# Performance work log

Measured on AMD Instinct MI355X. Metric: run time of the kernel, lower is better.

The kernel has to match this reference:

```python
import jax, jax.numpy as jnp
import numpy as np

B, S, IN, OUT = 4, 2048, 4096, 11008


def setup_inputs() -> dict:
    key = jax.random.key(0)
    k1, k2, k3, k4, k5 = jax.random.split(key, 5)
    x = jax.random.normal(k1, (B, S, IN), dtype=jnp.float32)
    # int8 quantized weights, stored as int32 per harness spec but values in int8 range
    W_int8 = jax.random.randint(k2, (OUT, IN), -128, 128, dtype=jnp.int32)
    # per-output-channel scales (small positive) and zero-points
    scale = jax.random.uniform(k3, (OUT,), dtype=jnp.float32, minval=1e-3, maxval=2e-2)
    zero = jax.random.uniform(k4, (OUT,), dtype=jnp.float32, minval=-8.0, maxval=8.0)
    bias = jax.random.normal(k5, (OUT,), dtype=jnp.float32) * 0.01
    return {"x": x, "W_int8": W_int8, "scale": scale, "zero": zero, "bias": bias}


def reference(x, W_int8, scale, zero, bias):
    # Original torch forward raises on NaN/Inf in x; for valid inputs the math is
    # quant_matmul: dequantize W = (W_int8 - zero) * scale (per output channel),
    # then y = x @ W.T + bias.
    W = (W_int8.astype(jnp.float32) - zero[:, None]) * scale[:, None]  # [OUT, IN]
    y = jnp.einsum('bsi,oi->bso', x, W) + bias  # [B, S, OUT]
    return y
```

## Files before the change

### kernel.cpp

```cpp
#include <hip/hip_runtime.h>
#include <stdint.h>


#define M_DIM 8192
#define N_DIM 11008
#define K_DIM 4096
#define NT    (K_DIM / 128)
#define BUFB  65536

typedef __attribute__((ext_vector_type(4))) int i32x4;


__global__ void convert_w_kernel(const int* __restrict__ w,
                                 int8_t* __restrict__ o, int n4) {
  int idx = blockIdx.x * blockDim.x + threadIdx.x;
  int stride = gridDim.x * blockDim.x;
  for (int i = idx; i < n4; i += stride) {
    int4 v = ((const int4*)w)[i];
    int r = (v.x & 255) | ((v.y & 255) << 8) | ((v.z & 255) << 16) | ((v.w & 255) << 24);
    ((int*)o)[i] = r;
  }
}

__global__ __launch_bounds__(256) void quantx_kernel(
    const float* __restrict__ x, int8_t* __restrict__ h8, int8_t* __restrict__ l8,
    float* __restrict__ xs, float* __restrict__ rsum) {
  const int row = blockIdx.x;
  const int t = threadIdx.x;
  const float4* px = (const float4*)(x + (size_t)row * K_DIM);
  float4 v[4];
  float mx = 0.f, sm = 0.f;
  #pragma unroll
  for (int i = 0; i < 4; ++i) {
    v[i] = px[i * 256 + t];
    mx = fmaxf(mx, fmaxf(fmaxf(fabsf(v[i].x), fabsf(v[i].y)),
                         fmaxf(fabsf(v[i].z), fabsf(v[i].w))));
    sm += v[i].x + v[i].y + v[i].z + v[i].w;
  }
  #pragma unroll
  for (int off = 32; off > 0; off >>= 1) {
    mx = fmaxf(mx, __shfl_down(mx, off));
    sm += __shfl_down(sm, off);
  }
  __shared__ float rmx[4], rsm[4];
  const int wv = t >> 6, ln = t & 63;
  if (ln == 0) { rmx[wv] = mx; rsm[wv] = sm; }
  __syncthreads();
  const float rowmax = fmaxf(fmaxf(rmx[0], rmx[1]), fmaxf(rmx[2], rmx[3]));
  if (t == 0) {
    xs[row] = rowmax > 0.f ? rowmax / 16256.f : 0.f;
    rsum[row] = rsm[0] + rsm[1] + rsm[2] + rsm[3];
  }
  const float inv = rowmax > 0.f ? 16256.f / rowmax : 0.f;
  int* hp = (int*)(h8 + (size_t)row * K_DIM);
  int* lp = (int*)(l8 + (size_t)row * K_DIM);
  #pragma unroll
  for (int i = 0; i < 4; ++i) {
    int q0 = (int)rintf(v[i].x * inv);
    int q1 = (int)rintf(v[i].y * inv);
    int q2 = (int)rintf(v[i].z * inv);
    int q3 = (int)rintf(v[i].w * inv);
    int h0 = (q0 + 64) >> 7, h1 = (q1 + 64) >> 7, h2 = (q2 + 64) >> 7, h3 = (q3 + 64) >> 7;
    int l0 = q0 - (h0 << 7), l1 = q1 - (h1 << 7), l2 = q2 - (h2 << 7), l3 = q3 - (h3 << 7);
    hp[i * 256 + t] = (h0 & 255) | ((h1 & 255) << 8) | ((h2 & 255) << 16) | ((h3 & 255) << 24);
    lp[i * 256 + t] = (l0 & 255) | ((l1 & 255) << 8) | ((l2 & 255) << 16) | ((l3 & 255) << 24);
  }
}


__device__ __forceinline__ void stage_A(
    const int8_t* __restrict__ Ah, const int8_t* __restrict__ Al,
    size_t a_base, int ks, int srow, int scol, int wave, int8_t* buf) {
  #pragma unroll
  for (int r = 0; r < 2; ++r) {
    const int8_t* g = Ah + a_base + (size_t)(r * 64 + srow) * K_DIM + ks + scol;
    __builtin_amdgcn_global_load_lds((const __attribute__((address_space(1))) void*)g,
        (__attribute__((address_space(3))) void*)(buf + r * 8192 + wave * 1024), 16, 0, 0);
  }
  #pragma unroll
  for (int r = 0; r < 2; ++r) {
    const int8_t* g = Al + a_base + (size_t)(r * 64 + srow) * K_DIM + ks + scol;
    __builtin_amdgcn_global_load_lds((const __attribute__((address_space(1))) void*)g,
        (__attribute__((address_space(3))) void*)(buf + 16384 + r * 8192 + wave * 1024), 16, 0, 0);
  }
}

__device__ __forceinline__ void stage_B(
    const int8_t* __restrict__ Bw, size_t b_base,
    int ks, int srow, int scol, int wave, int8_t* buf) {
  #pragma unroll
  for (int r = 0; r < 4; ++r) {
    const int8_t* g = Bw + b_base + (size_t)(r * 64 + srow) * K_DIM + ks + scol;
    __builtin_amdgcn_global_load_lds((const __attribute__((address_space(1))) void*)g,
        (__attribute__((address_space(3))) void*)(buf + 32768 + r * 8192 + wave * 1024), 16, 0, 0);
  }
}

__global__ __launch_bounds__(512, 2) void qgemm_kernel(
    const int8_t* __restrict__ Ah, const int8_t* __restrict__ Al,
    const int8_t* __restrict__ Bw, const float* __restrict__ xs,
    const float* __restrict__ rowsum, const float* __restrict__ scale,
    const float* __restrict__ zero, const float* __restrict__ bias,
    float* __restrict__ out) {
  extern __shared__ int8_t smem[];

  const int tid = threadIdx.x;
  const int wave = tid >> 6;
  const int lane = tid & 63;

  const int bid = blockIdx.x;
  const int wg = (bid & 7) * 344 + (bid >> 3);
  const int group = wg / 344;
  const int rem = wg % 344;
  const int bm = group * 8 + (rem & 7);
  const int bn = rem >> 3;

  const int wr = wave >> 2;
  const int wc = wave & 3;

  i32x4 acch[4][4], accl[4][4];
  #pragma unroll
  for (int i = 0; i < 4; ++i)
    #pragma unroll
    for (int j = 0; j < 4; ++j) {
      acch[i][j] = (i32x4){0, 0, 0, 0};
      accl[i][j] = (i32x4){0, 0, 0, 0};
    }

  const int srow = tid >> 3;
  const int scol = (((tid & 7) ^ ((tid >> 3) & 7)) << 4);
  const size_t a_base = (size_t)(bm * 128) * K_DIM;
  const size_t b_base = (size_t)((size_t)bn * 256) * K_DIM;

  const int fr = lane & 15;
  const int g = lane >> 4;
  const int sw = fr & 7;
  const int sc0 = ((g ^ sw) << 4);
  const int sc1 = (((g + 4) ^ sw) << 4);

  int arow[4], brow[4];
  #pragma unroll
  for (int i = 0; i < 4; ++i) {
    arow[i] = (wr * 64 + i * 16 + fr) * 128;
    brow[i] = (wc * 64 + i * 16 + fr) * 128;
  }

#define RD(sc, ldsAh_, ldsAl_, ldsB_, af, bf) do {                       \
    _Pragma("unroll")                                                    \
    for (int ni = 0; ni < 4; ++ni)                                       \
      bf[ni] = *(const i32x4*)((ldsB_) + brow[ni] + (sc));               \
    _Pragma("unroll")                                                    \
    for (int mi = 0; mi < 4; ++mi) {                                     \
      af[mi][0] = *(const i32x4*)((ldsAh_) + arow[mi] + (sc));           \
      af[mi][1] = *(const i32x4*)((ldsAl_) + arow[mi] + (sc));           \
    }                                                                    \
  } while (0)

#define MM(af, bf) do {                                                  \
    __builtin_amdgcn_s_setprio(1);                                       \
    _Pragma("unroll")                                                    \
    for (int mi = 0; mi < 4; ++mi)                                       \
      _Pragma("unroll")                                                  \
      for (int ni = 0; ni < 4; ++ni) {                                   \
        acch[mi][ni] = __builtin_amdgcn_mfma_i32_16x16x64_i8(af[mi][0], bf[ni], acch[mi][ni], 0, 0, 0); \
        accl[mi][ni] = __builtin_amdgcn_mfma_i32_16x16x64_i8(af[mi][1], bf[ni], accl[mi][ni], 0, 0, 0); \
      }                                                                  \
    __builtin_amdgcn_s_setprio(0);                                       \
  } while (0)

  i32x4 afA[4][2], bfA[4], afB[4][2], bfB[4];

  stage_A(Ah, Al, a_base, 0, srow, scol, wave, smem);
  stage_B(Bw, b_base, 0, srow, scol, wave, smem);
  asm volatile("s_waitcnt vmcnt(0)" ::: "memory");
  __builtin_amdgcn_s_barrier();
  {
    const int8_t* b0 = smem;
    RD(sc0, b0, b0 + 16384, b0 + 32768, afA, bfA);
  }

  #pragma unroll 1
  for (int t = 0; t < NT; ++t) {
    const int8_t* buf = smem + (t & 1) * BUFB;
    int8_t* nxt = smem + ((t + 1) & 1) * BUFB;
    const int8_t* ldsAh_ = buf;
    const int8_t* ldsAl_ = buf + 16384;
    const int8_t* ldsB_  = buf + 32768;
    const bool pf = (t + 1 < NT);
    const int nks = (t + 1) * 128;

    RD(sc1, ldsAh_, ldsAl_, ldsB_, afB, bfB);
    __builtin_amdgcn_sched_barrier(0);
    if (pf) stage_A(Ah, Al, a_base, nks, srow, scol, wave, nxt);

    MM(afA, bfA);

    if (pf) stage_B(Bw, b_base, nks, srow, scol, wave, nxt);
    __builtin_amdgcn_sched_barrier(0);

    MM(afB, bfB);

    asm volatile("s_waitcnt vmcnt(0)" ::: "memory");
    __builtin_amdgcn_s_barrier();

    if (pf) {
      const int8_t* nAh = nxt;
      const int8_t* nAl = nxt + 16384;
      const int8_t* nB  = nxt + 32768;
      RD(sc0, nAh, nAl, nB, afA, bfA);
    }
  }

#undef RD
#undef MM

  const int row0 = bm * 128 + wr * 64;
  const int col0 = bn * 256 + wc * 64;
  float s_[4], sz_[4], b_[4];
  #pragma unroll
  for (int ni = 0; ni < 4; ++ni) {
    const int n = col0 + ni * 16 + fr;
    const float s = scale[n];
    s_[ni] = s;
    sz_[ni] = s * zero[n];
    b_[ni] = bias[n];
  }
  #pragma unroll
  for (int mi = 0; mi < 4; ++mi) {
    #pragma unroll
    for (int j = 0; j < 4; ++j) {
      const int m = row0 + mi * 16 + g * 4 + j;
      const float xsm = xs[m];
      const float rs = rowsum[m];
      float* po = out + (size_t)m * N_DIM + col0;
      #pragma unroll
      for (int ni = 0; ni < 4; ++ni) {
        const float G = xsm * (128.f * (float)acch[mi][ni][j] + (float)accl[mi][ni][j]);
        po[ni * 16 + fr] = s_[ni] * G - sz_[ni] * rs + b_[ni];
      }
    }
  }
}


__global__ void fallback_kernel(const float* __restrict__ x, const int* __restrict__ w,
                                const float* __restrict__ scale, const float* __restrict__ zero,
                                const float* __restrict__ bias, float* __restrict__ out) {
  const int n = blockIdx.x * 16 + (threadIdx.x & 15);
  const int m = blockIdx.y * 16 + (threadIdx.x >> 4);
  const float z = zero[n];
  const float* xr = x + (size_t)m * K_DIM;
  const int* wr = w + (size_t)n * K_DIM;
  float acc = 0.f;
  for (int k = 0; k < K_DIM; ++k) acc += xr[k] * ((float)wr[k] - z);
  out[(size_t)m * N_DIM + n] = scale[n] * acc + bias[n];
}


extern "C" void kernel_launch(void* const* d_in, const int* in_sizes, int n_in,
                              void* d_out, int out_size, void* d_ws, size_t ws_size,
                              hipStream_t stream) {
  const float* x     = (const float*)d_in[0];
  const int*   w     = (const int*)d_in[1];
  const float* scale = (const float*)d_in[2];
  const float* zero  = (const float*)d_in[3];
  const float* bias  = (const float*)d_in[4];
  float* out = (float*)d_out;

  const size_t n_x = (size_t)M_DIM * K_DIM;
  const size_t n_w = (size_t)N_DIM * K_DIM;
  const size_t need = n_x * 2 + n_w + (size_t)M_DIM * 8;

  if (ws_size < need) {
    dim3 gr(N_DIM / 16, M_DIM / 16);
    fallback_kernel<<<gr, 256, 0, stream>>>(x, w, scale, zero, bias, out);
    return;
  }

  int8_t* x_h = (int8_t*)d_ws;
  int8_t* x_l = x_h + n_x;
  int8_t* w_8 = x_l + n_x;
  float* rsum = (float*)(w_8 + n_w);
  float* xs   = rsum + M_DIM;

  convert_w_kernel<<<2048, 256, 0, stream>>>(w, w_8, (int)(n_w / 4));
  quantx_kernel<<<M_DIM, 256, 0, stream>>>(x, x_h, x_l, xs, rsum);

  (void)hipFuncSetAttribute((const void*)qgemm_kernel,
                            hipFuncAttributeMaxDynamicSharedMemorySize, 2 * BUFB);

  const int nblocks = (M_DIM / 128) * (N_DIM / 256);
  qgemm_kernel<<<nblocks, 512, 2 * BUFB, stream>>>(x_h, x_l, w_8, xs, rsum,
                                                   scale, zero, bias, out);
}
```

Measured before the change: 764.7 us.

## Prepack weights into MFMA fragment layout and load B directly to registers

The weight conversion kernel now writes int8 weights pre-tiled in the exact per-lane MFMA B-fragment order. The GEMM then loads B straight from global memory into registers, one k-tile ahead, instead of staging it through LDS. This halves LDS use per buffer, which frees LDS capacity and removes LDS write/read traffic for B. The cost is that B global loads are no longer shared across waves in LDS; each wave fetches its own fragments, which raises L2 traffic. It also adds register pressure from the double-buffered B fragments and restructures the pipeline with partial vmcnt waits.

```diff
diff --git a/kernel.cpp b/kernel.cpp
--- a/kernel.cpp
+++ b/kernel.cpp
@@ -6,19 +6,29 @@
 #define N_DIM 11008
 #define K_DIM 4096
 #define NT    (K_DIM / 128)
-#define BUFB  65536
+#define BUFB  32768
 
 typedef __attribute__((ext_vector_type(4))) int i32x4;
 
 
-__global__ void convert_w_kernel(const int* __restrict__ w,
-                                 int8_t* __restrict__ o, int n4) {
-  int idx = blockIdx.x * blockDim.x + threadIdx.x;
-  int stride = gridDim.x * blockDim.x;
-  for (int i = idx; i < n4; i += stride) {
-    int4 v = ((const int4*)w)[i];
-    int r = (v.x & 255) | ((v.y & 255) << 8) | ((v.z & 255) << 16) | ((v.w & 255) << 24);
-    ((int*)o)[i] = r;
+__global__ __launch_bounds__(256) void convert_w_kernel(
+    const int* __restrict__ w, int8_t* __restrict__ Wq) {
+  const int q = blockIdx.x;
+  const int r = threadIdx.x & 15;
+  const int cg = threadIdx.x >> 4;
+  const int o = q * 16 + r;
+  const int4* src = (const int4*)(w + (size_t)o * K_DIM + cg * 256);
+  int8_t* dst = Wq + (size_t)q * 65536 + (size_t)(cg * 16) * 256 + r * 16;
+  #pragma unroll 4
+  for (int jc = 0; jc < 16; ++jc) {
+    int4 o4;
+    int4 v0 = src[jc * 4 + 0], v1 = src[jc * 4 + 1];
+    int4 v2 = src[jc * 4 + 2], v3 = src[jc * 4 + 3];
+    o4.x = (v0.x & 255) | ((v0.y & 255) << 8) | ((v0.z & 255) << 16) | ((v0.w & 255) << 24);
+    o4.y = (v1.x & 255) | ((v1.y & 255) << 8) | ((v1.z & 255) << 16) | ((v1.w & 255) << 24);
+    o4.z = (v2.x & 255) | ((v2.y & 255) << 8) | ((v2.z & 255) << 16) | ((v2.w & 255) << 24);
+    o4.w = (v3.x & 255) | ((v3.y & 255) << 8) | ((v3.z & 255) << 16) | ((v3.w & 255) << 24);
+    *(int4*)(dst + jc * 256) = o4;
   }
 }
 
@@ -85,20 +95,9 @@
   }
 }
 
-__device__ __forceinline__ void stage_B(
-    const int8_t* __restrict__ Bw, size_t b_base,
-    int ks, int srow, int scol, int wave, int8_t* buf) {
-  #pragma unroll
-  for (int r = 0; r < 4; ++r) {
-    const int8_t* g = Bw + b_base + (size_t)(r * 64 + srow) * K_DIM + ks + scol;
-    __builtin_amdgcn_global_load_lds((const __attribute__((address_space(1))) void*)g,
-        (__attribute__((address_space(3))) void*)(buf + 32768 + r * 8192 + wave * 1024), 16, 0, 0);
-  }
-}
-
 __global__ __launch_bounds__(512, 2) void qgemm_kernel(
     const int8_t* __restrict__ Ah, const int8_t* __restrict__ Al,
-    const int8_t* __restrict__ Bw, const float* __restrict__ xs,
+    const int8_t* __restrict__ Wq, const float* __restrict__ xs,
     const float* __restrict__ rowsum, const float* __restrict__ scale,
     const float* __restrict__ zero, const float* __restrict__ bias,
     float* __restrict__ out) {
@@ -130,89 +129,97 @@
   const int srow = tid >> 3;
   const int scol = (((tid & 7) ^ ((tid >> 3) & 7)) << 4);
   const size_t a_base = (size_t)(bm * 128) * K_DIM;
-  const size_t b_base = (size_t)((size_t)bn * 256) * K_DIM;
 
   const int fr = lane & 15;
   const int g = lane >> 4;
   const int sw = fr & 7;
   const int sc0 = ((g ^ sw) << 4);
   const int sc1 = (((g + 4) ^ sw) << 4);
-
-  int arow[4], brow[4];
-  #pragma unroll
-  for (int i = 0; i < 4; ++i) {
-    arow[i] = (wr * 64 + i * 16 + fr) * 128;
-    brow[i] = (wc * 64 + i * 16 + fr) * 128;
-  }
-
-#define RD(sc, ldsAh_, ldsAl_, ldsB_, af, bf) do {                       \
+  int arow[4];
+  #pragma unroll
+  for (int i = 0; i < 4; ++i) arow[i] = (wr * 64 + i * 16 + fr) * 128;
+
+  const uint32_t laneoff = (uint32_t)(g * 256 + fr * 16);
+  const int8_t* pb[4];
+  #pragma unroll
+  for (int ni = 0; ni < 4; ++ni)
+    pb[ni] = Wq + (size_t)((uint32_t)(bn * 16 + wc * 4 + ni) * 65536u + laneoff);
+
+#define LOADB(tt, bf) do {                                               \
     _Pragma("unroll")                                                    \
-    for (int ni = 0; ni < 4; ++ni)                                       \
-      bf[ni] = *(const i32x4*)((ldsB_) + brow[ni] + (sc));               \
+    for (int ni = 0; ni < 4; ++ni) {                                     \
+      bf[ni][0] = *(const i32x4*)(pb[ni] + (uint32_t)(tt) * 2048u);      \
+      bf[ni][1] = *(const i32x4*)(pb[ni] + (uint32_t)(tt) * 2048u + 1024u); \
+    }                                                                    \
+  } while (0)
+
+#define RDA(sc, pAh, pAl, af) do {                                       \
     _Pragma("unroll")                                                    \
     for (int mi = 0; mi < 4; ++mi) {                                     \
-      af[mi][0] = *(const i32x4*)((ldsAh_) + arow[mi] + (sc));           \
-      af[mi][1] = *(const i32x4*)((ldsAl_) + arow[mi] + (sc));           \
+      af[mi][0] = *(const i32x4*)((pAh) + arow[mi] + (sc));              \
+      af[mi][1] = *(const i32x4*)((pAl) + arow[mi] + (sc));              \
     }                                                                    \
   } while (0)
 
-#define MM(af, bf) do {                                                  \
+#define MMH(af, bf, hf) do {                                             \
     __builtin_amdgcn_s_setprio(1);                                       \
     _Pragma("unroll")                                                    \
     for (int mi = 0; mi < 4; ++mi)                                       \
       _Pragma("unroll")                                                  \
       for (int ni = 0; ni < 4; ++ni) {                                   \
-        acch[mi][ni] = __builtin_amdgcn_mfma_i32_16x16x64_i8(af[mi][0], bf[ni], acch[mi][ni], 0, 0, 0); \
-        accl[mi][ni] = __builtin_amdgcn_mfma_i32_16x16x64_i8(af[mi][1], bf[ni], accl[mi][ni], 0, 0, 0); \
+        acch[mi][ni] = __builtin_amdgcn_mfma_i32_16x16x64_i8(af[mi][0], bf[ni][hf], acch[mi][ni], 0, 0, 0); \
+        accl[mi][ni] = __builtin_amdgcn_mfma_i32_16x16x64_i8(af[mi][1], bf[ni][hf], accl[mi][ni], 0, 0, 0); \
       }                                                                  \
     __builtin_amdgcn_s_setprio(0);                                       \
   } while (0)
 
-  i32x4 afA[4][2], bfA[4], afB[4][2], bfB[4];
+  i32x4 bcur[4][2], bnxt[4][2], af[4][2];
 
   stage_A(Ah, Al, a_base, 0, srow, scol, wave, smem);
-  stage_B(Bw, b_base, 0, srow, scol, wave, smem);
-  asm volatile("s_waitcnt vmcnt(0)" ::: "memory");
-  __builtin_amdgcn_s_barrier();
-  {
-    const int8_t* b0 = smem;
-    RD(sc0, b0, b0 + 16384, b0 + 32768, afA, bfA);
-  }
+  __builtin_amdgcn_sched_barrier(0);
+  LOADB(0, bcur);
+  __builtin_amdgcn_sched_barrier(0);
 
   #pragma unroll 1
-  for (int t = 0; t < NT; ++t) {
+  for (int t = 0; t < NT - 1; ++t) {
     const int8_t* buf = smem + (t & 1) * BUFB;
     int8_t* nxt = smem + ((t + 1) & 1) * BUFB;
-    const int8_t* ldsAh_ = buf;
-    const int8_t* ldsAl_ = buf + 16384;
-    const int8_t* ldsB_  = buf + 32768;
-    const bool pf = (t + 1 < NT);
-    const int nks = (t + 1) * 128;
-
-    RD(sc1, ldsAh_, ldsAl_, ldsB_, afB, bfB);
+
+    stage_A(Ah, Al, a_base, (t + 1) * 128, srow, scol, wave, nxt);
     __builtin_amdgcn_sched_barrier(0);
-    if (pf) stage_A(Ah, Al, a_base, nks, srow, scol, wave, nxt);
-
-    MM(afA, bfA);
-
-    if (pf) stage_B(Bw, b_base, nks, srow, scol, wave, nxt);
+    LOADB(t + 1, bnxt);
     __builtin_amdgcn_sched_barrier(0);
 
-    MM(afB, bfB);
-
-    asm volatile("s_waitcnt vmcnt(0)" ::: "memory");
+    asm volatile("s_waitcnt vmcnt(20)" ::: "memory");
     __builtin_amdgcn_s_barrier();
 
-    if (pf) {
-      const int8_t* nAh = nxt;
-      const int8_t* nAl = nxt + 16384;
-      const int8_t* nB  = nxt + 32768;
-      RD(sc0, nAh, nAl, nB, afA, bfA);
+    RDA(sc0, buf, buf + 16384, af);
+    MMH(af, bcur, 0);
+    RDA(sc1, buf, buf + 16384, af);
+    MMH(af, bcur, 1);
+
+    __builtin_amdgcn_s_barrier();
+
+    #pragma unroll
+    for (int ni = 0; ni < 4; ++ni) {
+      bcur[ni][0] = bnxt[ni][0];
+      bcur[ni][1] = bnxt[ni][1];
     }
   }
 
-#undef RD
-#undef MM
+  {
+    const int8_t* buf = smem + ((NT - 1) & 1) * BUFB;
+    asm volatile("s_waitcnt vmcnt(8)" ::: "memory");
+    __builtin_amdgcn_s_barrier();
+    RDA(sc0, buf, buf + 16384, af);
+    MMH(af, bcur, 0);
+    RDA(sc1, buf, buf + 16384, af);
+    MMH(af, bcur, 1);
+  }
+
+#undef LOADB
+#undef RDA
+#undef MMH
 
   const int row0 = bm * 128 + wr * 64;
   const int col0 = bn * 256 + wc * 64;
@@ -279,17 +286,17 @@
 
   int8_t* x_h = (int8_t*)d_ws;
   int8_t* x_l = x_h + n_x;
-  int8_t* w_8 = x_l + n_x;
-  float* rsum = (float*)(w_8 + n_w);
+  int8_t* w_q = x_l + n_x;
+  float* rsum = (float*)(w_q + n_w);
   float* xs   = rsum + M_DIM;
 
-  convert_w_kernel<<<2048, 256, 0, stream>>>(w, w_8, (int)(n_w / 4));
+  convert_w_kernel<<<N_DIM / 16, 256, 0, stream>>>(w, w_q);
   quantx_kernel<<<M_DIM, 256, 0, stream>>>(x, x_h, x_l, xs, rsum);
 
   (void)hipFuncSetAttribute((const void*)qgemm_kernel,
                             hipFuncAttributeMaxDynamicSharedMemorySize, 2 * BUFB);
 
   const int nblocks = (M_DIM / 128) * (N_DIM / 256);
-  qgemm_kernel<<<nblocks, 512, 2 * BUFB, stream>>>(x_h, x_l, w_8, xs, rsum,
+  qgemm_kernel<<<nblocks, 512, 2 * BUFB, stream>>>(x_h, x_l, w_q, xs, rsum,
                                                    scale, zero, bias, out);
 }
```

Result: slower. 924.4 us (+20.9%).
